# Kernel tuning notes

Hardware: AMD Instinct MI355X
Metric: run time of the kernel (lower is better)

Reference implementation:

```python
import jax, jax.numpy as jnp
import numpy as np

N, M, FEAT, POS, D, MSG, NCLS = 64, 32, 256, 6, 262, 128, 7


def setup_inputs() -> dict:
    key = jax.random.key(0)
    ks = jax.random.split(key, 12)
    s = 0.05
    p = lambda k, shape: jax.random.normal(k, shape, jnp.float32) * s
    return {
        "nodes_feature": jax.random.normal(ks[0], (N, M, FEAT), jnp.float32),
        "pos": jax.random.normal(ks[1], (N, M, POS), jnp.float32),
        "num_rec": jax.random.randint(ks[2], (N,), 1, M + 1),
        "link_w1": p(ks[3], (D, 2 * D)),
        "link_b1": jnp.zeros((D,), jnp.float32),
        "link_w2": p(ks[4], (D,)),
        "link_b2": jnp.zeros((), jnp.float32),
        "msg_w": p(ks[5], (MSG, D)),
        "msg_b": jnp.zeros((MSG,), jnp.float32),
        "gru_w_ih": p(ks[6], (3 * D, MSG)),
        "gru_w_hh": p(ks[7], (3 * D, D)),
        "gru_b_ih": jnp.zeros((3 * D,), jnp.float32),
        "gru_b_hh": jnp.zeros((3 * D,), jnp.float32),
        "ro_w1": p(ks[8], (MSG, D)),
        "ro_b1": jnp.zeros((MSG,), jnp.float32),
        "ro_w2": p(ks[9], (NCLS, MSG)),
        "ro_b2": jnp.zeros((NCLS,), jnp.float32),
    }


def reference(nodes_feature, pos, num_rec, link_w1, link_b1, link_w2, link_b2,
              msg_w, msg_b, gru_w_ih, gru_w_hh, gru_b_ih, gru_b_hh,
              ro_w1, ro_b1, ro_w2, ro_b2):
    # node_feat = [resnet_feat, pos]  -> (N, M, 262)
    nf = jnp.concatenate([nodes_feature, pos], axis=-1)
    n, m, d = nf.shape
    valid = jnp.arange(m)[None, :] < num_rec[:, None]          # (N, M)
    pair = valid[:, :, None] & valid[:, None, :]               # (N, M, M)

    # edge_feat[b,:,i,j] = concat(nf[b,i], nf[b,j]); zero for invalid pairs
    ef = jnp.concatenate([
        jnp.broadcast_to(nf[:, :, None, :], (n, m, m, d)),
        jnp.broadcast_to(nf[:, None, :, :], (n, m, m, d)),
    ], axis=-1) * pair[..., None].astype(nf.dtype)             # (N, M, M, 2D)

    # 1x1 convs == per-pair MLP
    hlink = jax.nn.relu(jnp.einsum('bnwc,dc->bnwd', ef, link_w1) + link_b1)
    attmat = jax.nn.sigmoid(jnp.einsum('bnwd,d->bnw', hlink, link_w2) + link_b2)

    # messages are only summed over valid sender nodes w
    att_m = attmat * valid[:, None, :].astype(attmat.dtype)    # (N, M, M)

    def gru_step(x, h):
        # PyTorch GRU cell: gates order (r, z, n)
        gx = x @ gru_w_ih.T + gru_b_ih
        gh = h @ gru_w_hh.T + gru_b_hh
        xr, xz, xn = jnp.split(gx, 3, axis=-1)
        hr, hz, hn = jnp.split(gh, 3, axis=-1)
        r = jax.nn.sigmoid(xr + hr)
        z = jax.nn.sigmoid(xz + hz)
        c = jnp.tanh(xn + r * hn)
        return (1.0 - z) * c + z * h

    vmask = valid[..., None].astype(nf.dtype)
    h_state = nf                                               # pass 0 input state
    for _ in range(2):                                         # two message-passing rounds
        msg = h_state @ msg_w.T + msg_b                        # (N, M, 128)
        m_v = jnp.einsum('bnw,bwk->bnk', att_m, msg)           # attention-weighted sum
        h_state = gru_step(m_v, h_state) * vmask               # invalid nodes stay zero

    pred = (jax.nn.relu(h_state @ ro_w1.T + ro_b1) @ ro_w2.T + ro_b2) * vmask
    return pred, attmat
```

## Files before the change

kernel.cpp:

```cpp
#include <hip/hip_runtime.h>
#include <math.h>

#define N_G   64
#define M_N   32
#define FEAT  256
#define POSD  6
#define D     262
#define MSG   128
#define NCLS  7

#define KA_S  424
#define KHW   288
#define KFULL 416
#define PSTR  320

#define S_PROJ (528*288)
#define S_MSG  (128*288)
#define S_RZ   (544*416)
#define S_XN   (272*128)
#define S_HN   (272*288)
#define S_RO   (128*288)
#define S_RO2  (16*128)

#define O_WPROJ 0u
#define O_WMSG  76032u
#define O_WRZ   94464u
#define O_WXN   207616u
#define O_WHN   225024u
#define O_WRO   264192u
#define O_WRO2  282624u
#define O_GB    283648u

typedef __attribute__((ext_vector_type(8))) short short8;
typedef __attribute__((ext_vector_type(4))) short short4v;
typedef __attribute__((ext_vector_type(4))) float floatx4;

#define MFMA __builtin_amdgcn_mfma_f32_16x16x32_bf16

__device__ __forceinline__ short f2bf(float f) {
    union { float f; unsigned u; } v; v.f = f;
    unsigned r = v.u + 0x7FFF + ((v.u >> 16) & 1);
    return (short)(r >> 16);
}
__device__ __forceinline__ float bf2f(short s) {
    union { float f; unsigned u; } v;
    v.u = ((unsigned)(unsigned short)s) << 16;
    return v.f;
}
__device__ __forceinline__ float sigf(float x) {
    return __builtin_amdgcn_rcpf(1.f + __expf(-x));
}
__device__ __forceinline__ float tanh_fast(float x) {
    float e = __expf(-2.f * fabsf(x));
    float t = (1.f - e) * __builtin_amdgcn_rcpf(1.f + e);
    return copysignf(t, x);
}

__global__ __launch_bounds__(256) void prep_kernel(
    const float* __restrict__ w1, const float* __restrict__ msg_w,
    const float* __restrict__ w_ih, const float* __restrict__ w_hh,
    const float* __restrict__ ro_w1, const float* __restrict__ ro_w2,
    const float* __restrict__ b_ih, const float* __restrict__ b_hh,
    float* __restrict__ ws)
{
    short* wproj = (short*)(ws + O_WPROJ);
    short* wmsg  = (short*)(ws + O_WMSG);
    short* wrz   = (short*)(ws + O_WRZ);
    short* wxn   = (short*)(ws + O_WXN);
    short* whn   = (short*)(ws + O_WHN);
    short* wro   = (short*)(ws + O_WRO);
    short* wro2  = (short*)(ws + O_WRO2);
    float* gb    = ws + O_GB;

    int row = blockIdx.x * 4 + (threadIdx.x >> 6);
    const int lane = threadIdx.x & 63;
    if (row >= 1892) return;

    if (row < 528) {
        const int n = row;
        short* out = wproj + n * 288;
        const float* src = (n < D) ? (w1 + n * 524) : (w1 + (n - D) * 524 + D);
        for (int k = lane; k < 288; k += 64) {
            float v = (k < D && n < 524) ? src[k] : 0.f;
            out[k] = f2bf(v);
        }
        return;
    }
    row -= 528;
    if (row < 128) {
        const int n = row;
        short* out = wmsg + n * 288;
        const float* src = msg_w + n * D;
        for (int k = lane; k < 288; k += 64)
            out[k] = f2bf(k < D ? src[k] : 0.f);
        return;
    }
    row -= 128;
    if (row < 544) {
        const int g = row;
        const int gi = (g < 272) ? 0 : 1;
        const int d = g - gi * 272;
        short* out = wrz + g * 416;
        if (d < D) {
            const int r = gi * D + d;
            const float* sih = w_ih + r * MSG;
            const float* shh = w_hh + r * D - 128;
            for (int k = lane; k < 416; k += 64) {
                float v;
                if (k < 128)            v = sih[k];
                else if (k < 128 + D)   v = shh[k];
                else                    v = 0.f;
                out[k] = f2bf(v);
            }
        } else {
            for (int k = lane; k < 416; k += 64) out[k] = 0;
        }
        return;
    }
    row -= 544;
    if (row < 272) {
        const int d = row;
        short* out = wxn + d * 128;
        const float* src = w_ih + (2 * D + d) * MSG;
        for (int k = lane; k < 128; k += 64)
            out[k] = f2bf(d < D ? src[k] : 0.f);
        return;
    }
    row -= 272;
    if (row < 272) {
        const int d = row;
        short* out = whn + d * 288;
        const float* src = w_hh + (2 * D + d) * D;
        for (int k = lane; k < 288; k += 64)
            out[k] = f2bf((d < D && k < D) ? src[k] : 0.f);
        return;
    }
    row -= 272;
    if (row < 128) {
        const int n = row;
        short* out = wro + n * 288;
        const float* src = ro_w1 + n * D;
        for (int k = lane; k < 288; k += 64)
            out[k] = f2bf(k < D ? src[k] : 0.f);
        return;
    }
    row -= 128;
    if (row < 16) {
        const int n = row;
        short* out = wro2 + n * 128;
        const float* src = ro_w2 + n * MSG;
        for (int k = lane; k < 128; k += 64)
            out[k] = f2bf(n < NCLS ? src[k] : 0.f);
        return;
    }
    row -= 16;
    {
        const int seg = row;
        float* out = gb + seg * 272;
        for (int d = lane; d < 272; d += 64) {
            float v = 0.f;
            if (d < D) {
                if (seg == 0)      v = b_ih[d] + b_hh[d];
                else if (seg == 1) v = b_ih[D + d] + b_hh[D + d];
                else if (seg == 2) v = b_ih[2 * D + d];
                else               v = b_hh[2 * D + d];
            }
            out[d] = v;
        }
    }
}

__global__ __launch_bounds__(512, 2) void fused_kernel(
    const float* __restrict__ nodes, const float* __restrict__ pos,
    const int* __restrict__ nrec_g,
    const float* __restrict__ b1g, const float* __restrict__ w2g,
    const float* __restrict__ b2g, const float* __restrict__ msg_bg,
    const float* __restrict__ ro_b1g, const float* __restrict__ ro_b2g,
    const float* __restrict__ ws,
    float* __restrict__ att_out, float* __restrict__ pred)
{
    const short* Wproj = (const short*)(ws + O_WPROJ);
    const short* Wmsg  = (const short*)(ws + O_WMSG);
    const short* Wrz   = (const short*)(ws + O_WRZ);
    const short* Wxn   = (const short*)(ws + O_WXN);
    const short* Whn   = (const short*)(ws + O_WHN);
    const short* Wro   = (const short*)(ws + O_WRO);
    const short* Wro2  = (const short*)(ws + O_WRO2);
    const float* gb    = ws + O_GB;

    __shared__ __align__(16) short bufA[32 * KA_S];
    __shared__ __align__(16) short bufB[32 * KA_S];
    __shared__ __align__(16) short paL[32 * PSTR];
    __shared__ __align__(16) short pbL[32 * PSTR];
    __shared__ __align__(16) short attL[32 * 40];
    __shared__ __align__(16) short msgT[128 * 40];
    __shared__ __align__(16) short hidL[32 * 136];
    __shared__ __align__(16) float b1L[PSTR], w2L[PSTR];

    const int b = blockIdx.x;
    const int tid = threadIdx.x;
    const int wave = tid >> 6, lane = tid & 63;
    const int quad = lane >> 4, lrow = lane & 15;

    floatx4 prm[10];
    {
        const floatx4* pb = (const floatx4*)(ws + O_WRZ);
        const int base = wave * 64 + lane;
#pragma unroll
        for (int p = 0; p < 10; ++p)
            prm[p] = pb[(p * 512 + base) * 8];
    }
    short8 wvA[9];
    {
        const short* bw = Wproj + (wave * 16 + lrow) * KHW + quad * 8;
#pragma unroll
        for (int kk = 0; kk < 9; ++kk) wvA[kk] = *(const short8*)(bw + kk * 32);
    }

    const int nr = nrec_g[b];

    for (int idx = tid; idx < 32 * 64; idx += 512) {
        int w = idx >> 6, c4 = idx & 63;
        floatx4 v = *(const floatx4*)(nodes + ((size_t)(b * 32 + w)) * FEAT + c4 * 4);
        short4v s; s[0] = f2bf(v[0]); s[1] = f2bf(v[1]); s[2] = f2bf(v[2]); s[3] = f2bf(v[3]);
        *(short4v*)(bufA + w * KA_S + 128 + c4 * 4) = s;
    }
    for (int idx = tid; idx < 32 * POSD; idx += 512) {
        int w = idx / POSD, c = idx % POSD;
        bufA[w * KA_S + 128 + FEAT + c] = f2bf(pos[((size_t)(b * 32 + w)) * POSD + c]);
    }
    for (int idx = tid; idx < 32 * 34; idx += 512) {
        int w = idx / 34, c = idx % 34;
        bufA[w * KA_S + 390 + c] = 0;
        bufB[w * KA_S + 390 + c] = 0;
    }
    for (int idx = tid; idx < 32 * (PSTR - D); idx += 512) {
        int w = idx / (PSTR - D), c = idx % (PSTR - D);
        paL[w * PSTR + D + c] = 0;
        pbL[w * PSTR + D + c] = 0;
    }
    for (int d = tid; d < PSTR; d += 512) {
        b1L[d] = (d < D) ? b1g[d] : 0.f;
        w2L[d] = (d < D) ? w2g[d] : 0.f;
    }
#pragma unroll
    for (int p = 0; p < 10; ++p) asm volatile("" :: "v"(prm[p]));
    __syncthreads();

    {
        auto store_proj = [&](int s, floatx4 acc0, floatx4 acc1) {
            int col = s * 16 + lrow;
#pragma unroll
            for (int rr = 0; rr < 4; ++rr) {
                int r0 = quad * 4 + rr;
                if (col < D) {
                    paL[r0 * PSTR + col] = f2bf(acc0[rr]);
                    paL[(r0 + 16) * PSTR + col] = f2bf(acc1[rr]);
                } else if (col < 2 * D) {
                    pbL[r0 * PSTR + (col - D)] = f2bf(acc0[rr]);
                    pbL[(r0 + 16) * PSTR + (col - D)] = f2bf(acc1[rr]);
                }
            }
        };
        auto store_msg = [&](int s, floatx4 acc0, floatx4 acc1) {
            int col = (s - 33) * 16 + lrow;
            float bias = msg_bg[col];
#pragma unroll
            for (int rr = 0; rr < 4; ++rr) {
                msgT[col * 40 + quad * 4 + rr] = f2bf(acc0[rr] + bias);
                msgT[col * 40 + 16 + quad * 4 + rr] = f2bf(acc1[rr] + bias);
            }
        };

        short8 aF0[9], aF1[9];
        {
            const short* ap = bufA + lrow * KA_S + 128 + quad * 8;
#pragma unroll
            for (int kk = 0; kk < 9; ++kk) {
                aF0[kk] = *(const short8*)(ap + kk * 32);
                aF1[kk] = *(const short8*)(ap + 16 * KA_S + kk * 32);
            }
#pragma unroll
            for (int kk = 0; kk < 9; ++kk)
                asm volatile("" : "+v"(aF0[kk]), "+v"(aF1[kk]));
        }
        short8 wvB[9];

#define P1_LOAD(DST, TT) do { \
            const short* bw_ = ((TT) < 33) \
                ? Wproj + ((TT) * 16 + lrow) * KHW + quad * 8 \
                : Wmsg + (((TT) - 33) * 16 + lrow) * KHW + quad * 8; \
            _Pragma("unroll") \
            for (int kk = 0; kk < 9; ++kk) DST[kk] = *(const short8*)(bw_ + kk * 32); \
        } while (0)

#define P1_TILE(W, TT) do { \
            floatx4 acc0_ = {}, acc1_ = {}; \
            _Pragma("unroll") \
            for (int kk = 0; kk < 9; ++kk) { \
                acc0_ = MFMA(aF0[kk], W[kk], acc0_, 0, 0, 0); \
                acc1_ = MFMA(aF1[kk], W[kk], acc1_, 0, 0, 0); \
            } \
            if ((TT) < 33) store_proj((TT), acc0_, acc1_); \
            else store_msg((TT), acc0_, acc1_); \
        } while (0)

        int t = wave;
        P1_LOAD(wvB, t + 8);
        P1_TILE(wvA, t);
        t += 8;
        P1_LOAD(wvA, t + 8);
        P1_TILE(wvB, t);
        t += 8;
        P1_LOAD(wvB, t + 8);
        P1_TILE(wvA, t);
        t += 8;
        P1_LOAD(wvA, t + 8);
        P1_TILE(wvB, t);
        t += 8;
        if (t + 8 < 41) P1_LOAD(wvB, t + 8);
        P1_TILE(wvA, t);
        t += 8;
        if (t < 41) P1_TILE(wvB, t);
#undef P1_LOAD
#undef P1_TILE
    }
    __syncthreads();

    {
        const int grp = tid >> 4;
        const int c16 = tid & 15;
        const float b2v = b2g[0];
        float pav[5][4], b1v[5][4], w2v[5][4];
#pragma unroll
        for (int k = 0; k < 5; ++k) {
            int dbase = c16 * 4 + 64 * k;
            short4v p = *(const short4v*)(paL + grp * PSTR + dbase);
            floatx4 bb = *(const floatx4*)(b1L + dbase);
            floatx4 ww = *(const floatx4*)(w2L + dbase);
#pragma unroll
            for (int e = 0; e < 4; ++e) {
                pav[k][e] = bf2f(p[e]); b1v[k][e] = bb[e]; w2v[k][e] = ww[e];
            }
        }
        float p0 = 0.f;
#pragma unroll
        for (int k = 0; k < 5; ++k)
#pragma unroll
            for (int e = 0; e < 4; ++e)
                p0 += fmaxf(b1v[k][e], 0.f) * w2v[k][e];
        p0 += __shfl_down(p0, 8, 16); p0 += __shfl_down(p0, 4, 16);
        p0 += __shfl_down(p0, 2, 16); p0 += __shfl_down(p0, 1, 16);
        float c0 = sigf(p0 + b2v);
        const bool vi = grp < nr;
        for (int j = 0; j < 32; ++j) {
            float a;
            if (j < nr && vi) {
                const short* pb = pbL + j * PSTR + c16 * 4;
                float s = 0.f;
#pragma unroll
                for (int k = 0; k < 5; ++k) {
                    short4v q = *(const short4v*)(pb + 64 * k);
#pragma unroll
                    for (int e = 0; e < 4; ++e) {
                        float v = pav[k][e] + bf2f(q[e]) + b1v[k][e];
                        s += fmaxf(v, 0.f) * w2v[k][e];
                    }
                }
                s += __shfl_down(s, 8, 16); s += __shfl_down(s, 4, 16);
                s += __shfl_down(s, 2, 16); s += __shfl_down(s, 1, 16);
                a = sigf(s + b2v);
            } else {
                a = c0;
            }
            if (c16 == 0) {
                att_out[((size_t)(b * 32 + grp)) * 32 + j] = a;
                attL[grp * 40 + j] = f2bf((j < nr) ? a : 0.f);
            }
        }
    }
    __syncthreads();

    for (int rnd = 0; rnd < 2; ++rnd) {
        short* src = rnd ? bufB : bufA;
        short* dst = rnd ? bufA : bufB;

        if (rnd) {
            int s = wave;
            const short* bw = Wmsg + (s * 16 + lrow) * KHW + quad * 8;
            short8 wm[9];
#pragma unroll
            for (int kk = 0; kk < 9; ++kk) wm[kk] = *(const short8*)(bw + kk * 32);
            floatx4 acc0 = {}, acc1 = {};
            const short* ap = src + lrow * KA_S + 128 + quad * 8;
#pragma unroll
            for (int kk = 0; kk < 9; ++kk) {
                short8 x0 = *(const short8*)(ap + kk * 32);
                short8 x1 = *(const short8*)(ap + 16 * KA_S + kk * 32);
                acc0 = MFMA(x0, wm[kk], acc0, 0, 0, 0);
                acc1 = MFMA(x1, wm[kk], acc1, 0, 0, 0);
            }
            int col = s * 16 + lrow;
            float bias = msg_bg[col];
#pragma unroll
            for (int rr = 0; rr < 4; ++rr) {
                msgT[col * 40 + quad * 4 + rr] = f2bf(acc0[rr] + bias);
                msgT[col * 40 + 16 + quad * 4 + rr] = f2bf(acc1[rr] + bias);
            }
            __syncthreads();
        }

        {
            int mi = wave & 1, ng = wave >> 1;
            short8 afrag = *(const short8*)(attL + (mi * 16 + lrow) * 40 + quad * 8);
            floatx4 acc0 = {}, acc1 = {};
            short8 bf0 = *(const short8*)(msgT + (ng * 32 + lrow) * 40 + quad * 8);
            short8 bf1 = *(const short8*)(msgT + (ng * 32 + 16 + lrow) * 40 + quad * 8);
            acc0 = MFMA(afrag, bf0, acc0, 0, 0, 0);
            acc1 = MFMA(afrag, bf1, acc1, 0, 0, 0);
#pragma unroll
            for (int rr = 0; rr < 4; ++rr) {
                int m = mi * 16 + quad * 4 + rr;
                src[m * KA_S + ng * 32 + lrow] = f2bf(acc0[rr]);
                src[m * KA_S + ng * 32 + 16 + lrow] = f2bf(acc1[rr]);
            }
        }
        __syncthreads();

        {
            short8 aA0[13], aA1[13];
            {
                const short* ap0 = src + lrow * KA_S + quad * 8;
#pragma unroll
                for (int kk = 0; kk < 13; ++kk) {
                    aA0[kk] = *(const short8*)(ap0 + kk * 32);
                    aA1[kk] = *(const short8*)(ap0 + 16 * KA_S + kk * 32);
                }
#pragma unroll
                for (int kk = 0; kk < 13; ++kk)
                    asm volatile("" : "+v"(aA0[kk]), "+v"(aA1[kk]));
            }
            for (int s = wave; s < 17; s += 8) {
                const short* bpr = Wrz + (s * 16 + lrow) * KFULL + quad * 8;
                const short* bpz = bpr + 272 * KFULL;
                const short* bpx = Wxn + (s * 16 + lrow) * 128 + quad * 8;
                const short* bph = Whn + (s * 16 + lrow) * KHW + quad * 8;

                short8 wr[13];
#pragma unroll
                for (int kk = 0; kk < 13; ++kk) wr[kk] = *(const short8*)(bpr + kk * 32);
#pragma unroll
                for (int kk = 0; kk < 13; ++kk) asm volatile("" : "+v"(wr[kk]));

                floatx4 aR0 = {}, aR1 = {}, aZ0 = {}, aZ1 = {};
                floatx4 aN0 = {}, aN1 = {}, aH0 = {}, aH1 = {};
#pragma unroll
                for (int kk = 0; kk < 13; ++kk) {
                    aR0 = MFMA(aA0[kk], wr[kk], aR0, 0, 0, 0);
                    aR1 = MFMA(aA1[kk], wr[kk], aR1, 0, 0, 0);
                    if (kk < 4) {
                        short8 bx = *(const short8*)(bpx + kk * 32);
                        aN0 = MFMA(aA0[kk], bx, aN0, 0, 0, 0);
                        aN1 = MFMA(aA1[kk], bx, aN1, 0, 0, 0);
                    }
                    wr[kk] = *(const short8*)(bpz + kk * 32);
                }
#pragma unroll
                for (int kk = 0; kk < 13; ++kk) {
                    aZ0 = MFMA(aA0[kk], wr[kk], aZ0, 0, 0, 0);
                    aZ1 = MFMA(aA1[kk], wr[kk], aZ1, 0, 0, 0);
                    if (kk < 9) wr[kk] = *(const short8*)(bph + kk * 32);
                }
#pragma unroll
                for (int kk = 0; kk < 9; ++kk) {
                    aH0 = MFMA(aA0[kk + 4], wr[kk], aH0, 0, 0, 0);
                    aH1 = MFMA(aA1[kk + 4], wr[kk], aH1, 0, 0, 0);
                }

                int d = s * 16 + lrow;
                if (d < D) {
                    float bgr = gb[d], bgz = gb[272 + d];
                    float bxv = gb[544 + d], bhv = gb[816 + d];
#pragma unroll
                    for (int i = 0; i < 2; ++i) {
                        floatx4 vR = i ? aR1 : aR0, vZ = i ? aZ1 : aZ0;
                        floatx4 vN = i ? aN1 : aN0, vH = i ? aH1 : aH0;
#pragma unroll
                        for (int rr = 0; rr < 4; ++rr) {
                            int m = i * 16 + quad * 4 + rr;
                            float rg = sigf(vR[rr] + bgr);
                            float zg = sigf(vZ[rr] + bgz);
                            float cg = tanh_fast(vN[rr] + bxv + rg * (vH[rr] + bhv));
                            float hold = bf2f(src[m * KA_S + 128 + d]);
                            float hv = (1.f - zg) * cg + zg * hold;
                            if (m >= nr) hv = 0.f;
                            dst[m * KA_S + 128 + d] = f2bf(hv);
                        }
                    }
                }
            }
        }
        __syncthreads();
    }

    {
        int s = wave;
        const short* bw = Wro + (s * 16 + lrow) * KHW + quad * 8;
        short8 wv[9];
#pragma unroll
        for (int kk = 0; kk < 9; ++kk) wv[kk] = *(const short8*)(bw + kk * 32);
        floatx4 acc0 = {}, acc1 = {};
        const short* ap = bufA + lrow * KA_S + 128 + quad * 8;
#pragma unroll
        for (int kk = 0; kk < 9; ++kk) {
            short8 x0 = *(const short8*)(ap + kk * 32);
            short8 x1 = *(const short8*)(ap + 16 * KA_S + kk * 32);
            acc0 = MFMA(x0, wv[kk], acc0, 0, 0, 0);
            acc1 = MFMA(x1, wv[kk], acc1, 0, 0, 0);
        }
        int col = s * 16 + lrow;
        float bias = ro_b1g[col];
#pragma unroll
        for (int rr = 0; rr < 4; ++rr) {
            hidL[(quad * 4 + rr) * 136 + col] = f2bf(fmaxf(acc0[rr] + bias, 0.f));
            hidL[(16 + quad * 4 + rr) * 136 + col] = f2bf(fmaxf(acc1[rr] + bias, 0.f));
        }
    }
    __syncthreads();

    if (wave == 0) {
        const short* bw = Wro2 + lrow * 128 + quad * 8;
        short8 wv[4];
#pragma unroll
        for (int kk = 0; kk < 4; ++kk) wv[kk] = *(const short8*)(bw + kk * 32);
        floatx4 acc0 = {}, acc1 = {};
        const short* ap = hidL + lrow * 136 + quad * 8;
#pragma unroll
        for (int kk = 0; kk < 4; ++kk) {
            short8 x0 = *(const short8*)(ap + kk * 32);
            short8 x1 = *(const short8*)(ap + 16 * 136 + kk * 32);
            acc0 = MFMA(x0, wv[kk], acc0, 0, 0, 0);
            acc1 = MFMA(x1, wv[kk], acc1, 0, 0, 0);
        }
        int q = lrow;
        if (q < NCLS) {
            float bias = ro_b2g[q];
#pragma unroll
            for (int i = 0; i < 2; ++i) {
#pragma unroll
                for (int rr = 0; rr < 4; ++rr) {
                    int m = i * 16 + quad * 4 + rr;
                    float v = (i ? acc1[rr] : acc0[rr]) + bias;
                    if (m >= nr) v = 0.f;
                    pred[((size_t)(b * 32 + m)) * NCLS + q] = v;
                }
            }
        }
    }
}

extern "C" void kernel_launch(void* const* d_in, const int* in_sizes, int n_in,
                              void* d_out, int out_size, void* d_ws, size_t ws_size,
                              hipStream_t stream)
{
    const float* nodes = (const float*)d_in[0];
    const float* pos   = (const float*)d_in[1];
    const int*   nrec  = (const int*)d_in[2];
    const float* w1    = (const float*)d_in[3];
    const float* b1    = (const float*)d_in[4];
    const float* w2    = (const float*)d_in[5];
    const float* b2    = (const float*)d_in[6];
    const float* msg_w = (const float*)d_in[7];
    const float* msg_b = (const float*)d_in[8];
    const float* w_ih  = (const float*)d_in[9];
    const float* w_hh  = (const float*)d_in[10];
    const float* b_ih  = (const float*)d_in[11];
    const float* b_hh  = (const float*)d_in[12];
    const float* ro_w1 = (const float*)d_in[13];
    const float* ro_b1 = (const float*)d_in[14];
    const float* ro_w2 = (const float*)d_in[15];
    const float* ro_b2 = (const float*)d_in[16];
    float* ws   = (float*)d_ws;
    float* pred = (float*)d_out;
    float* attout = pred + (size_t)N_G * M_N * NCLS;

    prep_kernel<<<473, 256, 0, stream>>>(w1, msg_w, w_ih, w_hh, ro_w1, ro_w2,
                                         b_ih, b_hh, ws);
    fused_kernel<<<N_G, 512, 0, stream>>>(nodes, pos, nrec, b1, w2, b2, msg_b,
                                          ro_b1, ro_b2, ws, attout, pred);
}
```

Before: 148.8 us.

## Pre-swizzle bf16 weights into MFMA fragment order for contiguous per-wave loads

The prep kernel now writes each weight matrix in MFMA B-fragment order, with every (16-row tile, k-chunk) block stored as 512 contiguous shorts indexed by lane. The fused kernel's weight loads change from strided row-major addresses (stride 288/416/128) to fully contiguous 1 KB per-wave loads. The aim is to cut global/L2 transaction count and cache-line waste in the latency-bound weight streaming inside the fused kernel. In exchange, the prep kernel does scattered reads from the fp32 sources, and its grid size is recomputed to match.

```diff
diff --git a/kernel.cpp b/kernel.cpp
--- a/kernel.cpp
+++ b/kernel.cpp
@@ -10,17 +10,7 @@
 #define NCLS  7
 
 #define KA_S  424
-#define KHW   288
-#define KFULL 416
 #define PSTR  320
-
-#define S_PROJ (528*288)
-#define S_MSG  (128*288)
-#define S_RZ   (544*416)
-#define S_XN   (272*128)
-#define S_HN   (272*288)
-#define S_RO   (128*288)
-#define S_RO2  (16*128)
 
 #define O_WPROJ 0u
 #define O_WMSG  76032u
@@ -72,90 +62,115 @@
     short* wro2  = (short*)(ws + O_WRO2);
     float* gb    = ws + O_GB;
 
-    int row = blockIdx.x * 4 + (threadIdx.x >> 6);
+    int job = blockIdx.x * 4 + (threadIdx.x >> 6);
     const int lane = threadIdx.x & 63;
-    if (row >= 1892) return;
-
-    if (row < 528) {
-        const int n = row;
-        short* out = wproj + n * 288;
-        const float* src = (n < D) ? (w1 + n * 524) : (w1 + (n - D) * 524 + D);
-        for (int k = lane; k < 288; k += 64) {
-            float v = (k < D && n < 524) ? src[k] : 0.f;
-            out[k] = f2bf(v);
-        }
+    if (job >= 1112) return;
+    const int lrow = lane & 15, quad = lane >> 4;
+
+    if (job < 297) {
+        const int s = job / 9, kk = job % 9;
+        const int n = s * 16 + lrow, kb = quad * 8 + kk * 32;
+        short8 o;
+#pragma unroll
+        for (int e = 0; e < 8; ++e) {
+            int k = kb + e;
+            float v = 0.f;
+            if (k < D && n < 524)
+                v = (n < D) ? w1[n * 524 + k] : w1[(n - D) * 524 + D + k];
+            o[e] = f2bf(v);
+        }
+        *(short8*)(wproj + job * 512 + lane * 8) = o;
         return;
     }
-    row -= 528;
-    if (row < 128) {
-        const int n = row;
-        short* out = wmsg + n * 288;
-        const float* src = msg_w + n * D;
-        for (int k = lane; k < 288; k += 64)
-            out[k] = f2bf(k < D ? src[k] : 0.f);
+    job -= 297;
+    if (job < 72) {
+        const int s = job / 9, kk = job % 9;
+        const int n = s * 16 + lrow, kb = quad * 8 + kk * 32;
+        short8 o;
+#pragma unroll
+        for (int e = 0; e < 8; ++e) {
+            int k = kb + e;
+            o[e] = f2bf(k < D ? msg_w[n * D + k] : 0.f);
+        }
+        *(short8*)(wmsg + job * 512 + lane * 8) = o;
         return;
     }
-    row -= 128;
-    if (row < 544) {
-        const int g = row;
-        const int gi = (g < 272) ? 0 : 1;
-        const int d = g - gi * 272;
-        short* out = wrz + g * 416;
-        if (d < D) {
-            const int r = gi * D + d;
-            const float* sih = w_ih + r * MSG;
-            const float* shh = w_hh + r * D - 128;
-            for (int k = lane; k < 416; k += 64) {
-                float v;
-                if (k < 128)            v = sih[k];
-                else if (k < 128 + D)   v = shh[k];
-                else                    v = 0.f;
-                out[k] = f2bf(v);
-            }
-        } else {
-            for (int k = lane; k < 416; k += 64) out[k] = 0;
-        }
+    job -= 72;
+    if (job < 442) {
+        const int gi = job >= 221;
+        const int jj = job - gi * 221;
+        const int s = jj / 13, kk = jj % 13;
+        const int d = s * 16 + lrow, kb = quad * 8 + kk * 32;
+        short8 o;
+#pragma unroll
+        for (int e = 0; e < 8; ++e) {
+            int k = kb + e;
+            float v = 0.f;
+            if (d < D) {
+                int r = gi * D + d;
+                if (k < 128)          v = w_ih[r * MSG + k];
+                else if (k < 128 + D) v = w_hh[r * D + (k - 128)];
+            }
+            o[e] = f2bf(v);
+        }
+        *(short8*)(wrz + job * 512 + lane * 8) = o;
         return;
     }
-    row -= 544;
-    if (row < 272) {
-        const int d = row;
-        short* out = wxn + d * 128;
-        const float* src = w_ih + (2 * D + d) * MSG;
-        for (int k = lane; k < 128; k += 64)
-            out[k] = f2bf(d < D ? src[k] : 0.f);
+    job -= 442;
+    if (job < 68) {
+        const int s = job / 4, kk = job % 4;
+        const int d = s * 16 + lrow, kb = quad * 8 + kk * 32;
+        short8 o;
+#pragma unroll
+        for (int e = 0; e < 8; ++e) {
+            int k = kb + e;
+            o[e] = f2bf(d < D ? w_ih[(2 * D + d) * MSG + k] : 0.f);
+        }
+        *(short8*)(wxn + job * 512 + lane * 8) = o;
         return;
     }
-    row -= 272;
-    if (row < 272) {
-        const int d = row;
-        short* out = whn + d * 288;
-        const float* src = w_hh + (2 * D + d) * D;
-        for (int k = lane; k < 288; k += 64)
-            out[k] = f2bf((d < D && k < D) ? src[k] : 0.f);
+    job -= 68;
+    if (job < 153) {
+        const int s = job / 9, kk = job % 9;
+        const int d = s * 16 + lrow, kb = quad * 8 + kk * 32;
+        short8 o;
+#pragma unroll
+        for (int e = 0; e < 8; ++e) {
+            int k = kb + e;
+            o[e] = f2bf((d < D && k < D) ? w_hh[(2 * D + d) * D + k] : 0.f);
+        }
+        *(short8*)(whn + job * 512 + lane * 8) = o;
         return;
     }
-    row -= 272;
-    if (row < 128) {
-        const int n = row;
-        short* out = wro + n * 288;
-        const float* src = ro_w1 + n * D;
-        for (int k = lane; k < 288; k += 64)
-            out[k] = f2bf(k < D ? src[k] : 0.f);
+    job -= 153;
+    if (job < 72) {
+        const int s = job / 9, kk = job % 9;
+        const int n = s * 16 + lrow, kb = quad * 8 + kk * 32;
+        short8 o;
+#pragma unroll
+        for (int e = 0; e < 8; ++e) {
+            int k = kb + e;
+            o[e] = f2bf(k < D ? ro_w1[n * D + k] : 0.f);
+        }
+        *(short8*)(wro + job * 512 + lane * 8) = o;
         return;
     }
-    row -= 128;
-    if (row < 16) {
-        const int n = row;
-        short* out = wro2 + n * 128;
-        const float* src = ro_w2 + n * MSG;
-        for (int k = lane; k < 128; k += 64)
-            out[k] = f2bf(n < NCLS ? src[k] : 0.f);
+    job -= 72;
+    if (job < 4) {
+        const int kk = job;
+        const int n = lrow, kb = quad * 8 + kk * 32;
+        short8 o;
+#pragma unroll
+        for (int e = 0; e < 8; ++e) {
+            int k = kb + e;
+            o[e] = f2bf(n < NCLS ? ro_w2[n * MSG + k] : 0.f);
+        }
+        *(short8*)(wro2 + job * 512 + lane * 8) = o;
         return;
     }
-    row -= 16;
+    job -= 4;
     {
-        const int seg = row;
+        const int seg = job;
         float* out = gb + seg * 272;
         for (int d = lane; d < 272; d += 64) {
             float v = 0.f;
@@ -212,9 +227,9 @@
     }
     short8 wvA[9];
     {
-        const short* bw = Wproj + (wave * 16 + lrow) * KHW + quad * 8;
-#pragma unroll
-        for (int kk = 0; kk < 9; ++kk) wvA[kk] = *(const short8*)(bw + kk * 32);
+        const short* bw = Wproj + wave * 9 * 512 + lane * 8;
+#pragma unroll
+        for (int kk = 0; kk < 9; ++kk) wvA[kk] = *(const short8*)(bw + kk * 512);
     }
 
     const int nr = nrec_g[b];
@@ -288,10 +303,10 @@
 
 #define P1_LOAD(DST, TT) do { \
             const short* bw_ = ((TT) < 33) \
-                ? Wproj + ((TT) * 16 + lrow) * KHW + quad * 8 \
-                : Wmsg + (((TT) - 33) * 16 + lrow) * KHW + quad * 8; \
+                ? Wproj + (TT) * 9 * 512 + lane * 8 \
+                : Wmsg + ((TT) - 33) * 9 * 512 + lane * 8; \
             _Pragma("unroll") \
-            for (int kk = 0; kk < 9; ++kk) DST[kk] = *(const short8*)(bw_ + kk * 32); \
+            for (int kk = 0; kk < 9; ++kk) DST[kk] = *(const short8*)(bw_ + kk * 512); \
         } while (0)
 
 #define P1_TILE(W, TT) do { \
@@ -387,10 +402,10 @@
 
         if (rnd) {
             int s = wave;
-            const short* bw = Wmsg + (s * 16 + lrow) * KHW + quad * 8;
+            const short* bw = Wmsg + s * 9 * 512 + lane * 8;
             short8 wm[9];
 #pragma unroll
-            for (int kk = 0; kk < 9; ++kk) wm[kk] = *(const short8*)(bw + kk * 32);
+            for (int kk = 0; kk < 9; ++kk) wm[kk] = *(const short8*)(bw + kk * 512);
             floatx4 acc0 = {}, acc1 = {};
             const short* ap = src + lrow * KA_S + 128 + quad * 8;
 #pragma unroll
@@ -441,14 +456,14 @@
                     asm volatile("" : "+v"(aA0[kk]), "+v"(aA1[kk]));
             }
             for (int s = wave; s < 17; s += 8) {
-                const short* bpr = Wrz + (s * 16 + lrow) * KFULL + quad * 8;
-                const short* bpz = bpr + 272 * KFULL;
-                const short* bpx = Wxn + (s * 16 + lrow) * 128 + quad * 8;
-                const short* bph = Whn + (s * 16 + lrow) * KHW + quad * 8;
+                const short* bpr = Wrz + (s * 13) * 512 + lane * 8;
+                const short* bpz = Wrz + (221 + s * 13) * 512 + lane * 8;
+                const short* bpx = Wxn + (s * 4) * 512 + lane * 8;
+                const short* bph = Whn + (s * 9) * 512 + lane * 8;
 
                 short8 wr[13];
 #pragma unroll
-                for (int kk = 0; kk < 13; ++kk) wr[kk] = *(const short8*)(bpr + kk * 32);
+                for (int kk = 0; kk < 13; ++kk) wr[kk] = *(const short8*)(bpr + kk * 512);
 #pragma unroll
                 for (int kk = 0; kk < 13; ++kk) asm volatile("" : "+v"(wr[kk]));
 
@@ -459,17 +474,17 @@
                     aR0 = MFMA(aA0[kk], wr[kk], aR0, 0, 0, 0);
                     aR1 = MFMA(aA1[kk], wr[kk], aR1, 0, 0, 0);
                     if (kk < 4) {
-                        short8 bx = *(const short8*)(bpx + kk * 32);
+                        short8 bx = *(const short8*)(bpx + kk * 512);
                         aN0 = MFMA(aA0[kk], bx, aN0, 0, 0, 0);
                         aN1 = MFMA(aA1[kk], bx, aN1, 0, 0, 0);
                     }
-                    wr[kk] = *(const short8*)(bpz + kk * 32);
+                    wr[kk] = *(const short8*)(bpz + kk * 512);
                 }
 #pragma unroll
                 for (int kk = 0; kk < 13; ++kk) {
                     aZ0 = MFMA(aA0[kk], wr[kk], aZ0, 0, 0, 0);
                     aZ1 = MFMA(aA1[kk], wr[kk], aZ1, 0, 0, 0);
-                    if (kk < 9) wr[kk] = *(const short8*)(bph + kk * 32);
+                    if (kk < 9) wr[kk] = *(const short8*)(bph + kk * 512);
                 }
 #pragma unroll
                 for (int kk = 0; kk < 9; ++kk) {
@@ -505,10 +520,10 @@
 
     {
         int s = wave;
-        const short* bw = Wro + (s * 16 + lrow) * KHW + quad * 8;
+        const short* bw = Wro + s * 9 * 512 + lane * 8;
         short8 wv[9];
 #pragma unroll
-        for (int kk = 0; kk < 9; ++kk) wv[kk] = *(const short8*)(bw + kk * 32);
+        for (int kk = 0; kk < 9; ++kk) wv[kk] = *(const short8*)(bw + kk * 512);
         floatx4 acc0 = {}, acc1 = {};
         const short* ap = bufA + lrow * KA_S + 128 + quad * 8;
 #pragma unroll
@@ -529,10 +544,10 @@
     __syncthreads();
 
     if (wave == 0) {
-        const short* bw = Wro2 + lrow * 128 + quad * 8;
+        const short* bw = Wro2 + lane * 8;
         short8 wv[4];
 #pragma unroll
-        for (int kk = 0; kk < 4; ++kk) wv[kk] = *(const short8*)(bw + kk * 32);
+        for (int kk = 0; kk < 4; ++kk) wv[kk] = *(const short8*)(bw + kk * 512);
         floatx4 acc0 = {}, acc1 = {};
         const short* ap = hidL + lrow * 136 + quad * 8;
 #pragma unroll
@@ -584,7 +599,7 @@
     float* pred = (float*)d_out;
     float* attout = pred + (size_t)N_G * M_N * NCLS;
 
-    prep_kernel<<<473, 256, 0, stream>>>(w1, msg_w, w_ih, w_hh, ro_w1, ro_w2,
+    prep_kernel<<<278, 256, 0, stream>>>(w1, msg_w, w_ih, w_hh, ro_w1, ro_w2,
                                          b_ih, b_hh, ws);
     fused_kernel<<<N_G, 512, 0, stream>>>(nodes, pos, nrec, b1, w2, b2, msg_b,
                                           ro_b1, ro_b2, ws, attout, pred);
```

Measured after the change: 137.4 us, median of 3. -7.7%, faster.
